# Kernel tuning notes

Measured on AMD Instinct MI355X. Metric: run time of the kernel, lower is better.

Reference implementation:

```python
import jax, jax.numpy as jnp
import numpy as np

N_TRIAL = 1_000_000
N_STIM = 10_000
N_DIM = 16
N_GROUP = 4
N_REF = 8  # row = 1 query + 8 references
BETA = 1.0
GAMMA = 0.001
N_SELECT = np.array([1, 2, 3, 1], dtype=np.int32)  # per-config n_select (config_list)


def setup_inputs() -> dict:
    key = jax.random.key(0)
    k1, k2, k3, k4, k5 = jax.random.split(key, 5)
    stimulus_set = jax.random.randint(k1, (N_TRIAL, N_REF + 1), 0, N_STIM, dtype=jnp.int64)
    config_idx = jax.random.randint(k2, (N_TRIAL,), 0, len(N_SELECT), dtype=jnp.int64)
    group_id = jax.random.randint(k3, (N_TRIAL,), 0, N_GROUP, dtype=jnp.int64)
    is_present = jnp.ones((N_TRIAL, N_REF + 1), dtype=jnp.int32)
    embed_z = jax.random.normal(k4, (N_STIM, N_DIM), dtype=jnp.float32)
    attention_w = jax.random.uniform(k5, (N_GROUP, N_DIM), dtype=jnp.float32)
    return {
        "stimulus_set": stimulus_set,
        "config_idx": config_idx,
        "group_id": group_id,
        "is_present": is_present,
        "embed_z": embed_z,
        "attention_w": attention_w,
    }


def reference(stimulus_set, config_idx, group_id, is_present, embed_z, attention_w):
    # coordinate: embedding lookup -> (T, R+1, D)
    z = embed_z[stimulus_set]
    z_q = z[:, :1, :]   # (T, 1, D)
    z_r = z[:, 1:, :]   # (T, R, D)
    # attention: per-group dimension weights -> (T, 1, D)
    w = attention_w[group_id][:, None, :]
    # kernel: attention-weighted Minkowski (rho=2) distance + exponential similarity
    d = jnp.sqrt(jnp.sum(w * (z_q - z_r) ** 2, axis=-1))  # (T, R)
    sim_qr = jnp.exp(-BETA * d) + GAMMA
    # mask absent references (is_present[:, 1:])
    sim_qr = sim_qr * is_present[:, 1:].astype(sim_qr.dtype)
    # Ranked-sequence (Luce choice) probability, vectorized over all configs:
    # seq_prob = prod_{j < n_select} sim[:, j] / sum_{i >= j} sim[:, i]
    suffix = jnp.cumsum(sim_qr[:, ::-1], axis=1)[:, ::-1]  # (T, R) suffix sums
    n_select = jnp.asarray(N_SELECT)[config_idx]           # (T,)
    mask = jnp.arange(N_REF)[None, :] < n_select[:, None]  # (T, R)
    denom = jnp.where(mask, suffix, 1.0)
    prob = jnp.where(mask, sim_qr / denom, 1.0)
    likelihood = jnp.prod(prob, axis=1)  # (T,)
    return likelihood
```

## Files before the change

kernel.cpp:

```cpp
#include <hip/hip_runtime.h>
#include <math.h>

#define N_TRIAL 1000000
#define N_REF 8
#define N_DIM 16
#define N_GROUP 4
#define BETA 1.0f
#define GAMMA 0.001f
#define N_SELECT_PACKED 0x1321

#define WPB 4
#define D2_STRIDE 72

typedef float v4f  __attribute__((ext_vector_type(4)));
typedef int   v4iu __attribute__((ext_vector_type(4), aligned(4)));

__global__ __launch_bounds__(256) void likelihood_kernel(
    const int* __restrict__ stim,
    const int* __restrict__ config,
    const int* __restrict__ group,
    const int* __restrict__ present,
    const float* __restrict__ embed,
    const float* __restrict__ attw,
    float* __restrict__ out)
{
    __shared__ int4  s_stim4[WPB][144];
    __shared__ float s_d2[WPB][N_REF][D2_STRIDE];

    const int tid  = threadIdx.x;
    const int wv   = tid >> 6;
    const int lane = tid & 63;
    const int q    = lane >> 2;
    const int s    = lane & 3;

    int wtb = blockIdx.x * 256 + wv * 64;
    const bool valid = (wtb + lane) < N_TRIAL;
    if (wtb > N_TRIAL - 64) wtb = N_TRIAL - 64;

    {
        const int4* g4 = (const int4*)(stim + wtb * 9);
        s_stim4[wv][lane]      = g4[lane];
        s_stim4[wv][64 + lane] = g4[64 + lane];
        if (lane < 16) s_stim4[wv][128 + lane] = g4[128 + lane];
    }

    const int t2 = wtb + lane;
    const int* pp = present + t2 * 9;
    v4iu p0 = *(const v4iu*)(pp + 1);
    v4iu p1 = *(const v4iu*)(pp + 5);
    int  c    = config[t2];
    int  gall = group[t2];

    const float* embed_s = embed + s * 4;

    for (int j = 0; j < 4; ++j) {
        const int* sp = (const int*)&s_stim4[wv][0] + (16 * j + q) * 9;
        int idx[9];
#pragma unroll
        for (int i = 0; i < 9; ++i) idx[i] = sp[i];

        int g  = __shfl(gall, 16 * j + q);
        v4f w  = *(const v4f*)(attw + g * N_DIM + s * 4);
        v4f zq = *(const v4f*)(embed_s + idx[0] * N_DIM);

        float d2v[N_REF];
#pragma unroll
        for (int r = 0; r < N_REF; ++r) {
            v4f zr = *(const v4f*)(embed_s + idx[1 + r] * N_DIM);
            v4f dd = zq - zr;
            v4f wd = w * dd;
            float d2 = (wd.x * dd.x + wd.y * dd.y) + (wd.z * dd.z + wd.w * dd.w);
            d2 += __shfl_xor(d2, 1);
            d2 += __shfl_xor(d2, 2);
            d2v[r] = d2;
        }
        float da = (s == 0) ? d2v[0] : (s == 1) ? d2v[2] : (s == 2) ? d2v[4] : d2v[6];
        float db = (s == 0) ? d2v[1] : (s == 1) ? d2v[3] : (s == 2) ? d2v[5] : d2v[7];
        s_d2[wv][2 * s    ][16 * j + q] = da;
        s_d2[wv][2 * s + 1][16 * j + q] = db;
    }

    int pr[N_REF] = {p0.x, p0.y, p0.z, p0.w, p1.x, p1.y, p1.z, p1.w};

    float sim[N_REF];
#pragma unroll
    for (int r = 0; r < N_REF; ++r) {
        float d2 = s_d2[wv][r][lane];
        sim[r] = (__expf(-BETA * sqrtf(d2)) + GAMMA) * (float)pr[r];
    }

    int ns = (N_SELECT_PACKED >> ((c & 3) * 4)) & 0xF;

    float suf2 = sim[7];
#pragma unroll
    for (int r = 6; r >= 2; --r) suf2 += sim[r];
    float suf1 = suf2 + sim[1];
    float suf0 = suf1 + sim[0];

    float num = sim[0] * ((ns >= 2) ? sim[1] : 1.0f) * ((ns >= 3) ? sim[2] : 1.0f);
    float den = suf0   * ((ns >= 2) ? suf1   : 1.0f) * ((ns >= 3) ? suf2   : 1.0f);

    if (valid)
        out[wtb + lane] = __fdividef(num, den);
}

extern "C" void kernel_launch(void* const* d_in, const int* in_sizes, int n_in,
                              void* d_out, int out_size, void* d_ws, size_t ws_size,
                              hipStream_t stream) {
    const int*   stim    = (const int*)d_in[0];
    const int*   config  = (const int*)d_in[1];
    const int*   group   = (const int*)d_in[2];
    const int*   present = (const int*)d_in[3];
    const float* embed   = (const float*)d_in[4];
    const float* attw    = (const float*)d_in[5];
    float*       out     = (float*)d_out;

    int blocks = (N_TRIAL + 255) / 256;
    likelihood_kernel<<<blocks, 256, 0, stream>>>(stim, config, group, present,
                                                  embed, attw, out);
}
```

Measured before the change: 139.8 us.

## Double-buffer embedding gathers across trial groups and stage presence mask in LDS

Restructures the per-wave loop over four 16-trial groups into a software-pipelined sequence: all nine embedding rows for the next group are gathered into registers while the current group is computed. The is_present rows are now loaded into shared memory with coalesced int4 loads instead of strided per-thread loads. The four attention-weight rows are preloaded and selected by group id. Launch bounds add a minimum of 3 blocks per CU. The intent is to hide gather latency and get better memory coalescing, at the cost of higher register pressure and extra LDS use.

```diff
diff --git a/kernel.cpp b/kernel.cpp
--- a/kernel.cpp
+++ b/kernel.cpp
@@ -12,10 +12,9 @@
 #define WPB 4
 #define D2_STRIDE 72
 
-typedef float v4f  __attribute__((ext_vector_type(4)));
-typedef int   v4iu __attribute__((ext_vector_type(4), aligned(4)));
+typedef float v4f __attribute__((ext_vector_type(4)));
 
-__global__ __launch_bounds__(256) void likelihood_kernel(
+__global__ __launch_bounds__(256, 3) void likelihood_kernel(
     const int* __restrict__ stim,
     const int* __restrict__ config,
     const int* __restrict__ group,
@@ -25,6 +24,7 @@
     float* __restrict__ out)
 {
     __shared__ int4  s_stim4[WPB][144];
+    __shared__ int4  s_pres4[WPB][144];
     __shared__ float s_d2[WPB][N_REF][D2_STRIDE];
 
     const int tid  = threadIdx.x;
@@ -42,32 +42,44 @@
         s_stim4[wv][lane]      = g4[lane];
         s_stim4[wv][64 + lane] = g4[64 + lane];
         if (lane < 16) s_stim4[wv][128 + lane] = g4[128 + lane];
+        const int4* p4 = (const int4*)(present + wtb * 9);
+        s_pres4[wv][lane]      = p4[lane];
+        s_pres4[wv][64 + lane] = p4[64 + lane];
+        if (lane < 16) s_pres4[wv][128 + lane] = p4[128 + lane];
     }
 
     const int t2 = wtb + lane;
-    const int* pp = present + t2 * 9;
-    v4iu p0 = *(const v4iu*)(pp + 1);
-    v4iu p1 = *(const v4iu*)(pp + 5);
-    int  c    = config[t2];
-    int  gall = group[t2];
+    int c    = config[t2];
+    int gall = group[t2];
 
-    const float* embed_s = embed + s * 4;
+    v4f wt0 = *(const v4f*)(attw + 0 * N_DIM + s * 4);
+    v4f wt1 = *(const v4f*)(attw + 1 * N_DIM + s * 4);
+    v4f wt2 = *(const v4f*)(attw + 2 * N_DIM + s * 4);
+    v4f wt3 = *(const v4f*)(attw + 3 * N_DIM + s * 4);
 
-    for (int j = 0; j < 4; ++j) {
-        const int* sp = (const int*)&s_stim4[wv][0] + (16 * j + q) * 9;
-        int idx[9];
+    const float* embed_s  = embed + s * 4;
+    const int*   stim_lds = (const int*)&s_stim4[wv][0];
+
+    v4f z0[9], z1[9];
+    int idx[9];
+
 #pragma unroll
-        for (int i = 0; i < 9; ++i) idx[i] = sp[i];
+    for (int i = 0; i < 9; ++i) idx[i] = stim_lds[(16 * 0 + q) * 9 + i];
+#pragma unroll
+    for (int i = 0; i < 9; ++i) z0[i] = *(const v4f*)(embed_s + idx[i] * N_DIM);
+#pragma unroll
+    for (int i = 0; i < 9; ++i) idx[i] = stim_lds[(16 * 1 + q) * 9 + i];
+#pragma unroll
+    for (int i = 0; i < 9; ++i) z1[i] = *(const v4f*)(embed_s + idx[i] * N_DIM);
 
-        int g  = __shfl(gall, 16 * j + q);
-        v4f w  = *(const v4f*)(attw + g * N_DIM + s * 4);
-        v4f zq = *(const v4f*)(embed_s + idx[0] * N_DIM);
-
+    auto compute = [&](int j, v4f* z) {
+        int g = __shfl(gall, 16 * j + q);
+        v4f w = (g == 0) ? wt0 : (g == 1) ? wt1 : (g == 2) ? wt2 : wt3;
+        v4f zq = z[0];
         float d2v[N_REF];
 #pragma unroll
         for (int r = 0; r < N_REF; ++r) {
-            v4f zr = *(const v4f*)(embed_s + idx[1 + r] * N_DIM);
-            v4f dd = zq - zr;
+            v4f dd = zq - z[1 + r];
             v4f wd = w * dd;
             float d2 = (wd.x * dd.x + wd.y * dd.y) + (wd.z * dd.z + wd.w * dd.w);
             d2 += __shfl_xor(d2, 1);
@@ -78,15 +90,28 @@
         float db = (s == 0) ? d2v[1] : (s == 1) ? d2v[3] : (s == 2) ? d2v[5] : d2v[7];
         s_d2[wv][2 * s    ][16 * j + q] = da;
         s_d2[wv][2 * s + 1][16 * j + q] = db;
-    }
+    };
 
-    int pr[N_REF] = {p0.x, p0.y, p0.z, p0.w, p1.x, p1.y, p1.z, p1.w};
+    compute(0, z0);
+#pragma unroll
+    for (int i = 0; i < 9; ++i) idx[i] = stim_lds[(16 * 2 + q) * 9 + i];
+#pragma unroll
+    for (int i = 0; i < 9; ++i) z0[i] = *(const v4f*)(embed_s + idx[i] * N_DIM);
+    compute(1, z1);
+#pragma unroll
+    for (int i = 0; i < 9; ++i) idx[i] = stim_lds[(16 * 3 + q) * 9 + i];
+#pragma unroll
+    for (int i = 0; i < 9; ++i) z1[i] = *(const v4f*)(embed_s + idx[i] * N_DIM);
+    compute(2, z0);
+    compute(3, z1);
+
+    const int* pres_lds = (const int*)&s_pres4[wv][0] + lane * 9;
 
     float sim[N_REF];
 #pragma unroll
     for (int r = 0; r < N_REF; ++r) {
         float d2 = s_d2[wv][r][lane];
-        sim[r] = (__expf(-BETA * sqrtf(d2)) + GAMMA) * (float)pr[r];
+        sim[r] = (__expf(-BETA * sqrtf(d2)) + GAMMA) * (float)pres_lds[1 + r];
     }
 
     int ns = (N_SELECT_PACKED >> ((c & 3) * 4)) & 0xF;
```

Result: slower. 144.5 us (+3.4%).

## Gather embeddings as bf16 from a converted table and stage presence in LDS

Applied to the files above, without the earlier changes.

A small pre-kernel rounds the embedding table to bf16 into workspace, and the main kernel gathers 8-byte bf16 quads per lane instead of 16-byte float4, expanding them back to fp32. This halves the bytes fetched by the random gathers. The presence mask is now loaded coalesced into shared memory alongside the stimulus indices instead of as strided per-thread vector loads. It adds an extra kernel launch and lowers embedding precision to bf16, which changes numerical results slightly.

```diff
diff --git a/kernel.cpp b/kernel.cpp
--- a/kernel.cpp
+++ b/kernel.cpp
@@ -2,6 +2,7 @@
 #include <math.h>
 
 #define N_TRIAL 1000000
+#define N_STIM 10000
 #define N_REF 8
 #define N_DIM 16
 #define N_GROUP 4
@@ -12,19 +13,40 @@
 #define WPB 4
 #define D2_STRIDE 72
 
-typedef float v4f  __attribute__((ext_vector_type(4)));
-typedef int   v4iu __attribute__((ext_vector_type(4), aligned(4)));
+typedef float v4f __attribute__((ext_vector_type(4)));
+
+__global__ __launch_bounds__(256) void convert_kernel(
+    const float* __restrict__ embed, unsigned int* __restrict__ ebf)
+{
+    int i = blockIdx.x * 256 + threadIdx.x;
+    if (i >= N_STIM * N_DIM / 2) return;
+    unsigned int b0 = __builtin_bit_cast(unsigned int, embed[2 * i]);
+    unsigned int b1 = __builtin_bit_cast(unsigned int, embed[2 * i + 1]);
+    b0 = (b0 + 0x7fffu + ((b0 >> 16) & 1u)) >> 16;
+    b1 = (b1 + 0x7fffu + ((b1 >> 16) & 1u)) >> 16;
+    ebf[i] = b0 | (b1 << 16);
+}
+
+__device__ __forceinline__ v4f bf16x4_to_f32(uint2 u) {
+    v4f z;
+    z.x = __builtin_bit_cast(float, u.x << 16);
+    z.y = __builtin_bit_cast(float, u.x & 0xffff0000u);
+    z.z = __builtin_bit_cast(float, u.y << 16);
+    z.w = __builtin_bit_cast(float, u.y & 0xffff0000u);
+    return z;
+}
 
 __global__ __launch_bounds__(256) void likelihood_kernel(
     const int* __restrict__ stim,
     const int* __restrict__ config,
     const int* __restrict__ group,
     const int* __restrict__ present,
-    const float* __restrict__ embed,
+    const uint2* __restrict__ ebf,
     const float* __restrict__ attw,
     float* __restrict__ out)
 {
     __shared__ int4  s_stim4[WPB][144];
+    __shared__ int4  s_pres4[WPB][144];
     __shared__ float s_d2[WPB][N_REF][D2_STRIDE];
 
     const int tid  = threadIdx.x;
@@ -42,31 +64,33 @@
         s_stim4[wv][lane]      = g4[lane];
         s_stim4[wv][64 + lane] = g4[64 + lane];
         if (lane < 16) s_stim4[wv][128 + lane] = g4[128 + lane];
+        const int4* p4 = (const int4*)(present + wtb * 9);
+        s_pres4[wv][lane]      = p4[lane];
+        s_pres4[wv][64 + lane] = p4[64 + lane];
+        if (lane < 16) s_pres4[wv][128 + lane] = p4[128 + lane];
     }
 
     const int t2 = wtb + lane;
-    const int* pp = present + t2 * 9;
-    v4iu p0 = *(const v4iu*)(pp + 1);
-    v4iu p1 = *(const v4iu*)(pp + 5);
-    int  c    = config[t2];
-    int  gall = group[t2];
+    int c    = config[t2];
+    int gall = group[t2];
 
-    const float* embed_s = embed + s * 4;
+    const uint2* ebf_s   = ebf + s;
+    const int*   stim_lds = (const int*)&s_stim4[wv][0];
 
     for (int j = 0; j < 4; ++j) {
-        const int* sp = (const int*)&s_stim4[wv][0] + (16 * j + q) * 9;
+        const int* sp = stim_lds + (16 * j + q) * 9;
         int idx[9];
 #pragma unroll
         for (int i = 0; i < 9; ++i) idx[i] = sp[i];
 
         int g  = __shfl(gall, 16 * j + q);
         v4f w  = *(const v4f*)(attw + g * N_DIM + s * 4);
-        v4f zq = *(const v4f*)(embed_s + idx[0] * N_DIM);
+        v4f zq = bf16x4_to_f32(ebf_s[idx[0] * 4]);
 
         float d2v[N_REF];
 #pragma unroll
         for (int r = 0; r < N_REF; ++r) {
-            v4f zr = *(const v4f*)(embed_s + idx[1 + r] * N_DIM);
+            v4f zr = bf16x4_to_f32(ebf_s[idx[1 + r] * 4]);
             v4f dd = zq - zr;
             v4f wd = w * dd;
             float d2 = (wd.x * dd.x + wd.y * dd.y) + (wd.z * dd.z + wd.w * dd.w);
@@ -80,13 +104,13 @@
         s_d2[wv][2 * s + 1][16 * j + q] = db;
     }
 
-    int pr[N_REF] = {p0.x, p0.y, p0.z, p0.w, p1.x, p1.y, p1.z, p1.w};
+    const int* pres_lds = (const int*)&s_pres4[wv][0] + lane * 9;
 
     float sim[N_REF];
 #pragma unroll
     for (int r = 0; r < N_REF; ++r) {
         float d2 = s_d2[wv][r][lane];
-        sim[r] = (__expf(-BETA * sqrtf(d2)) + GAMMA) * (float)pr[r];
+        sim[r] = (__expf(-BETA * sqrtf(d2)) + GAMMA) * (float)pres_lds[1 + r];
     }
 
     int ns = (N_SELECT_PACKED >> ((c & 3) * 4)) & 0xF;
@@ -115,7 +139,12 @@
     const float* attw    = (const float*)d_in[5];
     float*       out     = (float*)d_out;
 
+    unsigned int* ebf = (unsigned int*)d_ws;
+
+    int cblocks = (N_STIM * N_DIM / 2 + 255) / 256;
+    convert_kernel<<<cblocks, 256, 0, stream>>>(embed, ebf);
+
     int blocks = (N_TRIAL + 255) / 256;
     likelihood_kernel<<<blocks, 256, 0, stream>>>(stim, config, group, present,
-                                                  embed, attw, out);
+                                                  (const uint2*)ebf, attw, out);
 }
```

Measured after the change: 144.2 us. 3.1% more time.
